# Kernel optimization log

Measured on AMD Instinct MI355X. Metric: run time of the kernel, lower is better.

The kernel has to match this reference:

```python
import jax, jax.numpy as jnp
import numpy as np

N = 20000
E = 320000
D = 512
H = 512


def _gcn_norm(edge_index, num_nodes):
    # PyG GCNConv: add self-loops, then sym-normalize with in-degree of A+I
    src = jnp.concatenate([edge_index[0], jnp.arange(num_nodes)])
    dst = jnp.concatenate([edge_index[1], jnp.arange(num_nodes)])
    deg = jax.ops.segment_sum(jnp.ones_like(dst, dtype=jnp.float32), dst, num_segments=num_nodes)
    dinv = jnp.where(deg > 0, jax.lax.rsqrt(deg), 0.0)
    norm = dinv[src] * dinv[dst]  # [E+N]
    return src, dst, norm


def _gcn_layer(x, src, dst, norm, W, b, num_nodes):
    h = x @ W                          # [N, out]
    msg = h[src] * norm[:, None]       # gather + scale, [E+N, out]
    out = jax.ops.segment_sum(msg, dst, num_segments=num_nodes)  # scatter-add
    return out + b


def setup_inputs() -> dict:
    key = jax.random.key(0)
    ks = jax.random.split(key, 8)
    features = jax.random.normal(ks[0], (N, D), dtype=jnp.float32)
    edge_index = jax.random.randint(ks[1], (2, E), 0, N, dtype=jnp.int64)
    edge_attr = jax.random.normal(ks[2], (E, 1), dtype=jnp.float32)  # unused by GCNConv
    s1 = 1.0 / np.sqrt(D)
    s2 = 1.0 / np.sqrt(H)
    W1 = jax.random.uniform(ks[3], (D, H), dtype=jnp.float32, minval=-s1, maxval=s1)
    b1 = jnp.zeros((H,), dtype=jnp.float32)
    W2 = jax.random.uniform(ks[4], (H, H), dtype=jnp.float32, minval=-s2, maxval=s2)
    b2 = jnp.zeros((H,), dtype=jnp.float32)
    return {"features": features, "edge_index": edge_index, "edge_attr": edge_attr,
            "W1": W1, "b1": b1, "W2": W2, "b2": b2}


def reference(features, edge_index, edge_attr, W1, b1, W2, b2):
    src, dst, norm = _gcn_norm(edge_index, N)
    x = jax.nn.relu(_gcn_layer(features, src, dst, norm, W1, b1, N))
    x = jax.nn.relu(_gcn_layer(x, src, dst, norm, W2, b2, N))
    # global_max_pool over the single graph (batch = all zeros) -> [1, H]
    return jnp.max(x, axis=0, keepdims=True)
```

## Files before the change

### kernel.cpp

```cpp
#include <hip/hip_runtime.h>

#define N_NODES 20000
#define MP      20096
#define N_EDGES 320000
#define DIM     512
#define SCAN_BLOCKS 79
#define FILL_BLOCKS 1250
#define W_BLOCKS    512
#define SORT_BLOCKS 79
#define NBIN 4096
#define MAXP_BLOCKS 256
#define MAXP_ROWS   79

typedef _Float16 half8 __attribute__((ext_vector_type(8)));
typedef float floatx4 __attribute__((ext_vector_type(4)));

#define GLD16(g, l) __builtin_amdgcn_global_load_lds( \
    (const __attribute__((address_space(1))) unsigned int*)(g), \
    (__attribute__((address_space(3))) unsigned int*)(l), 16, 0, 0)

__device__ inline void store8(_Float16* p, const float* v) {
    half8 o;
#pragma unroll
    for (int i = 0; i < 8; ++i) o[i] = (_Float16)v[i];
    *(half8*)p = o;
}
__device__ inline void store8(float* p, const float* v) {
    *(float4*)&p[0] = make_float4(v[0], v[1], v[2], v[3]);
    *(float4*)&p[4] = make_float4(v[4], v[5], v[6], v[7]);
}

__global__ void k_count(const int* __restrict__ dst, int* __restrict__ cnt) {
    int e = blockIdx.x * blockDim.x + threadIdx.x;
    if (e < N_EDGES) atomicAdd(&cnt[dst[e]], 1);
}

__global__ __launch_bounds__(256) void k_scan_a(const int* __restrict__ cnt,
                                                int* __restrict__ bsum) {
    __shared__ int buf[256];
    int gi = blockIdx.x * 256 + threadIdx.x;
    buf[threadIdx.x] = (gi < N_NODES) ? cnt[gi] : 0;
    __syncthreads();
    for (int off = 128; off > 0; off >>= 1) {
        if (threadIdx.x < off) buf[threadIdx.x] += buf[threadIdx.x + off];
        __syncthreads();
    }
    if (threadIdx.x == 0) bsum[blockIdx.x] = buf[0];
}

__global__ __launch_bounds__(128) void k_scan_b(const int* __restrict__ bsum,
                                                int* __restrict__ bbase) {
    __shared__ int buf[128];
    int tid = threadIdx.x;
    int v = (tid < SCAN_BLOCKS) ? bsum[tid] : 0;
    buf[tid] = v;
    __syncthreads();
    for (int off = 1; off < 128; off <<= 1) {
        int t = (tid >= off) ? buf[tid - off] : 0;
        __syncthreads();
        buf[tid] += t;
        __syncthreads();
    }
    if (tid < SCAN_BLOCKS) bbase[tid] = buf[tid] - v;
}

__global__ __launch_bounds__(256) void k_scan_c(const int* __restrict__ cnt,
                                                const int* __restrict__ bbase,
                                                int* __restrict__ offs,
                                                int* __restrict__ cursor,
                                                float* __restrict__ dinv,
                                                int* __restrict__ hist) {
    __shared__ int buf[256];
    __shared__ int lh[NBIN];
    int tid = threadIdx.x;
#pragma unroll
    for (int k = 0; k < NBIN / 256; ++k) lh[tid + k * 256] = 0;
    int gi = blockIdx.x * 256 + tid;
    int v = (gi < N_NODES) ? cnt[gi] : 0;
    buf[tid] = v;
    __syncthreads();
    for (int off = 1; off < 256; off <<= 1) {
        int t = (tid >= off) ? buf[tid - off] : 0;
        __syncthreads();
        buf[tid] += t;
        __syncthreads();
    }
    int base = bbase[blockIdx.x];
    if (gi < N_NODES) {
        int incl = base + buf[tid];
        offs[gi + 1] = incl;
        cursor[gi] = incl - v;
        dinv[gi] = rsqrtf((float)v + 1.0f);
        if (gi == 0) offs[0] = 0;
        int bin = (v > 255 ? 255 : v) * 16 + (gi & 15);
        atomicAdd(&lh[bin], 1);
    } else if (gi < MP) {
        dinv[gi] = 0.f;
    }
    __syncthreads();
#pragma unroll
    for (int k = 0; k < NBIN / 256; ++k) {
        int b2 = tid + k * 256;
        if (lh[b2]) atomicAdd(&hist[b2], lh[b2]);
    }
}

__global__ __launch_bounds__(256) void k_prep(const int* __restrict__ src,
                                              const int* __restrict__ dst,
                                              int* __restrict__ cursor,
                                              int* __restrict__ csr_src,
                                              const float* __restrict__ W1,
                                              const float* __restrict__ W2,
                                              _Float16* __restrict__ Wt1,
                                              _Float16* __restrict__ Wt2,
                                              const int* __restrict__ cnt,
                                              const int* __restrict__ hist,
                                              int* __restrict__ bincur,
                                              int* __restrict__ sorted) {
    int b = blockIdx.x;
    if (b < FILL_BLOCKS) {
        int e = b * 256 + threadIdx.x;
        int d = dst[e];
        int pos = atomicAdd(&cursor[d], 1);
        csr_src[pos] = src[e];
        return;
    }
    if (b < FILL_BLOCKS + W_BLOCKS) {
        int local = b - FILL_BLOCKS;
        int z = local >> 8, t = local & 255;
        const float* W = z ? W2 : W1;
        _Float16* Wt = z ? Wt2 : Wt1;
        __shared__ float tile[32][33];
        int bx = (t & 15) * 32, by = (t >> 4) * 32;
        int x = threadIdx.x & 31, y4 = (threadIdx.x >> 5) * 4;
#pragma unroll
        for (int r = 0; r < 4; ++r)
            tile[y4 + r][x] = W[(size_t)(by + y4 + r) * DIM + bx + x];
        __syncthreads();
#pragma unroll
        for (int r = 0; r < 4; ++r)
            Wt[(size_t)(bx + y4 + r) * DIM + by + x] = (_Float16)tile[x][y4 + r];
        return;
    }
    int sb = b - (FILL_BLOCKS + W_BLOCKS);
    __shared__ int sc[NBIN];
    __shared__ int ps[256];
    int tid = threadIdx.x;
    int tsum = 0;
#pragma unroll
    for (int k = 0; k < NBIN / 256; ++k) {
        int h = hist[tid * (NBIN / 256) + k];
        sc[tid * (NBIN / 256) + k] = tsum;
        tsum += h;
    }
    ps[tid] = tsum;
    __syncthreads();
    for (int off = 1; off < 256; off <<= 1) {
        int t = (tid >= off) ? ps[tid - off] : 0;
        __syncthreads();
        ps[tid] += t;
        __syncthreads();
    }
    int gbase = ps[tid] - tsum;
#pragma unroll
    for (int k = 0; k < NBIN / 256; ++k) sc[tid * (NBIN / 256) + k] += gbase;
    __syncthreads();
    int gi = sb * 256 + tid;
    if (gi < N_NODES) {
        int d = cnt[gi];
        int bin = (d > 255 ? 255 : d) * 16 + (gi & 15);
        int pos = sc[bin] + atomicAdd(&bincur[bin], 1);
        sorted[pos] = gi;
    } else if (gi < MP) {
        sorted[gi] = gi;
    }
}

__global__ __launch_bounds__(256) void k_gemm_f16(const _Float16* __restrict__ A,
                                                  const _Float16* __restrict__ Bt,
                                                  const float* __restrict__ dinv,
                                                  _Float16* __restrict__ G) {
    __shared__ _Float16 As[128 * 32];
    __shared__ _Float16 Bs[128 * 32];

    int t = threadIdx.x;
    int w = t >> 6, lane = t & 63;
    int lm = lane & 15, quad = lane >> 4;
    int m0 = blockIdx.x * 128, n0 = blockIdx.y * 128;
    int wm = (w & 1) * 64, wn = (w >> 1) * 64;

    floatx4 acc[4][4];
#pragma unroll
    for (int i = 0; i < 4; ++i)
#pragma unroll
        for (int j = 0; j < 4; ++j) acc[i][j] = (floatx4){0.f, 0.f, 0.f, 0.f};

    for (int k0 = 0; k0 < DIM; k0 += 32) {
        __syncthreads();
#pragma unroll
        for (int i = 0; i < 2; ++i) {
            int s = i * 256 + t;
            int m = s >> 2, kk = (s & 3) * 8;
            GLD16(A + (size_t)(m0 + m) * DIM + k0 + kk, As + s * 8);
            GLD16(Bt + (size_t)(n0 + m) * DIM + k0 + kk, Bs + s * 8);
        }
        __syncthreads();

        half8 af[4], bf[4];
#pragma unroll
        for (int i = 0; i < 4; ++i)
            af[i] = *(const half8*)&As[(wm + i * 16 + lm) * 32 + quad * 8];
#pragma unroll
        for (int j = 0; j < 4; ++j)
            bf[j] = *(const half8*)&Bs[(wn + j * 16 + lm) * 32 + quad * 8];
#pragma unroll
        for (int i = 0; i < 4; ++i)
#pragma unroll
            for (int j = 0; j < 4; ++j)
                acc[i][j] = __builtin_amdgcn_mfma_f32_16x16x32_f16(af[i], bf[j], acc[i][j], 0, 0, 0);
    }

#pragma unroll
    for (int i = 0; i < 4; ++i)
#pragma unroll
        for (int r = 0; r < 4; ++r) {
            int row = m0 + wm + i * 16 + quad * 4 + r;
            float dd = dinv[row];
#pragma unroll
            for (int j = 0; j < 4; ++j) {
                int col = n0 + wn + j * 16 + lm;
                G[(size_t)row * DIM + col] = (_Float16)(dd * acc[i][j][r]);
            }
        }
}

__global__ __launch_bounds__(256) void k_gemm_f32A(const float* __restrict__ A,
                                                   const _Float16* __restrict__ Bt,
                                                   const float* __restrict__ dinv,
                                                   _Float16* __restrict__ G) {
    __shared__ _Float16 As[128 * 32];
    __shared__ _Float16 Bs[128 * 32];

    int t = threadIdx.x;
    int w = t >> 6, lane = t & 63;
    int lm = lane & 15, quad = lane >> 4;
    int m0 = blockIdx.x * 128, n0 = blockIdx.y * 128;
    int wm = (w & 1) * 64, wn = (w >> 1) * 64;

    floatx4 acc[4][4];
#pragma unroll
    for (int i = 0; i < 4; ++i)
#pragma unroll
        for (int j = 0; j < 4; ++j) acc[i][j] = (floatx4){0.f, 0.f, 0.f, 0.f};

    for (int k0 = 0; k0 < DIM; k0 += 32) {
        __syncthreads();
#pragma unroll
        for (int i = 0; i < 2; ++i) {
            int s = i * 256 + t;
            int m = s >> 2, kk = (s & 3) * 8;
            GLD16(Bt + (size_t)(n0 + m) * DIM + k0 + kk, Bs + s * 8);
        }
#pragma unroll
        for (int i = 0; i < 2; ++i) {
            int s = i * 256 + t;
            int m = s >> 2, kk = (s & 3) * 8;
            int arow = m0 + m;
            half8 h;
            if (arow < N_NODES) {
                float4 a0 = *(const float4*)&A[(size_t)arow * DIM + k0 + kk];
                float4 a1 = *(const float4*)&A[(size_t)arow * DIM + k0 + kk + 4];
                h[0] = (_Float16)a0.x; h[1] = (_Float16)a0.y;
                h[2] = (_Float16)a0.z; h[3] = (_Float16)a0.w;
                h[4] = (_Float16)a1.x; h[5] = (_Float16)a1.y;
                h[6] = (_Float16)a1.z; h[7] = (_Float16)a1.w;
            } else {
#pragma unroll
                for (int q = 0; q < 8; ++q) h[q] = (_Float16)0.f;
            }
            *(half8*)&As[s * 8] = h;
        }
        __syncthreads();

        half8 af[4], bf[4];
#pragma unroll
        for (int i = 0; i < 4; ++i)
            af[i] = *(const half8*)&As[(wm + i * 16 + lm) * 32 + quad * 8];
#pragma unroll
        for (int j = 0; j < 4; ++j)
            bf[j] = *(const half8*)&Bs[(wn + j * 16 + lm) * 32 + quad * 8];
#pragma unroll
        for (int i = 0; i < 4; ++i)
#pragma unroll
            for (int j = 0; j < 4; ++j)
                acc[i][j] = __builtin_amdgcn_mfma_f32_16x16x32_f16(af[i], bf[j], acc[i][j], 0, 0, 0);
    }

#pragma unroll
    for (int i = 0; i < 4; ++i)
#pragma unroll
        for (int r = 0; r < 4; ++r) {
            int row = m0 + wm + i * 16 + quad * 4 + r;
            float dd = dinv[row];
#pragma unroll
            for (int j = 0; j < 4; ++j) {
                int col = n0 + wn + j * 16 + lm;
                G[(size_t)row * DIM + col] = (_Float16)(dd * acc[i][j][r]);
            }
        }
}

template <typename OutT>
__global__ __launch_bounds__(256) void k_agg_t(const _Float16* __restrict__ g,
                                               const float* __restrict__ dinv,
                                               const int* __restrict__ offs,
                                               const int* __restrict__ csr_src,
                                               const int* __restrict__ sorted,
                                               const float* __restrict__ bias,
                                               OutT* __restrict__ out) {
    int chunk = blockIdx.x & 7;
    int grp = blockIdx.x >> 3;
    int w = threadIdx.x >> 6, lane = threadIdx.x & 63;
    int slot = lane >> 3, fg = lane & 7;
    int idx = grp * 32 + w * 8 + slot;
    int node = sorted[idx];
    if ((unsigned)node >= (unsigned)MP) return;
    int fbase = chunk * 64 + fg * 8;
    size_t obase = (size_t)node * DIM + fbase;

    if (node >= N_NODES) {
        float z[8] = {0.f, 0.f, 0.f, 0.f, 0.f, 0.f, 0.f, 0.f};
        store8(&out[obase], z);
        return;
    }

    float acc[8];
    half8 self = *(const half8*)&g[obase];
#pragma unroll
    for (int i = 0; i < 8; ++i) acc[i] = (float)self[i];

    int beg = offs[node], end = offs[node + 1];
    int e = beg;
    for (; e + 8 <= end; e += 8) {
        int s0 = csr_src[e],     s1 = csr_src[e + 1], s2 = csr_src[e + 2], s3 = csr_src[e + 3];
        int s4 = csr_src[e + 4], s5 = csr_src[e + 5], s6 = csr_src[e + 6], s7 = csr_src[e + 7];
        half8 v0 = *(const half8*)&g[(size_t)s0 * DIM + fbase];
        half8 v1 = *(const half8*)&g[(size_t)s1 * DIM + fbase];
        half8 v2 = *(const half8*)&g[(size_t)s2 * DIM + fbase];
        half8 v3 = *(const half8*)&g[(size_t)s3 * DIM + fbase];
        half8 v4 = *(const half8*)&g[(size_t)s4 * DIM + fbase];
        half8 v5 = *(const half8*)&g[(size_t)s5 * DIM + fbase];
        half8 v6 = *(const half8*)&g[(size_t)s6 * DIM + fbase];
        half8 v7 = *(const half8*)&g[(size_t)s7 * DIM + fbase];
#pragma unroll
        for (int i = 0; i < 8; ++i)
            acc[i] += (((float)v0[i] + (float)v1[i]) + ((float)v2[i] + (float)v3[i])) +
                      (((float)v4[i] + (float)v5[i]) + ((float)v6[i] + (float)v7[i]));
    }
    for (; e + 4 <= end; e += 4) {
        int s0 = csr_src[e], s1 = csr_src[e + 1], s2 = csr_src[e + 2], s3 = csr_src[e + 3];
        half8 v0 = *(const half8*)&g[(size_t)s0 * DIM + fbase];
        half8 v1 = *(const half8*)&g[(size_t)s1 * DIM + fbase];
        half8 v2 = *(const half8*)&g[(size_t)s2 * DIM + fbase];
        half8 v3 = *(const half8*)&g[(size_t)s3 * DIM + fbase];
#pragma unroll
        for (int i = 0; i < 8; ++i)
            acc[i] += ((float)v0[i] + (float)v1[i]) + ((float)v2[i] + (float)v3[i]);
    }
    for (; e < end; ++e) {
        int s = csr_src[e];
        half8 v = *(const half8*)&g[(size_t)s * DIM + fbase];
#pragma unroll
        for (int i = 0; i < 8; ++i) acc[i] += (float)v[i];
    }

    float dd = dinv[node];
    float4 b0 = *(const float4*)&bias[fbase];
    float4 b1 = *(const float4*)&bias[fbase + 4];
    float bb[8] = {b0.x, b0.y, b0.z, b0.w, b1.x, b1.y, b1.z, b1.w};
    float o[8];
#pragma unroll
    for (int i = 0; i < 8; ++i) o[i] = fmaxf(fmaf(dd, acc[i], bb[i]), 0.f);
    store8(&out[obase], o);
}

__global__ __launch_bounds__(256) void k_maxpool(const float* __restrict__ x,
                                                 float* __restrict__ out) {
    __shared__ float lmax[4][DIM];
    int stream = threadIdx.x >> 6, lane = threadIdx.x & 63;
    int f0 = lane * 8;
    int r0 = blockIdx.x * MAXP_ROWS;
    int r1 = min(r0 + MAXP_ROWS, N_NODES);

    float m[8];
#pragma unroll
    for (int i = 0; i < 8; ++i) m[i] = 0.f;
    for (int r = r0 + stream; r < r1; r += 4) {
        float4 a = *(const float4*)&x[(size_t)r * DIM + f0];
        float4 b = *(const float4*)&x[(size_t)r * DIM + f0 + 4];
        m[0] = fmaxf(m[0], a.x); m[1] = fmaxf(m[1], a.y);
        m[2] = fmaxf(m[2], a.z); m[3] = fmaxf(m[3], a.w);
        m[4] = fmaxf(m[4], b.x); m[5] = fmaxf(m[5], b.y);
        m[6] = fmaxf(m[6], b.z); m[7] = fmaxf(m[7], b.w);
    }
#pragma unroll
    for (int i = 0; i < 8; ++i) lmax[stream][f0 + i] = m[i];
    __syncthreads();
#pragma unroll
    for (int rep = 0; rep < 2; ++rep) {
        int f = rep * 256 + threadIdx.x;
        float v = fmaxf(fmaxf(lmax[0][f], lmax[1][f]), fmaxf(lmax[2][f], lmax[3][f]));
        atomicMax((int*)&out[f], __float_as_int(v));
    }
}

extern "C" void kernel_launch(void* const* d_in, const int* in_sizes, int n_in,
                              void* d_out, int out_size, void* d_ws, size_t ws_size,
                              hipStream_t stream) {
    const float* features = (const float*)d_in[0];
    const int*   ei       = (const int*)d_in[1];
    const float* W1       = (const float*)d_in[3];
    const float* b1       = (const float*)d_in[4];
    const float* W2       = (const float*)d_in[5];
    const float* b2       = (const float*)d_in[6];
    float* out = (float*)d_out;

    const int* src = ei;
    const int* dst = ei + N_EDGES;

    char* p = (char*)d_ws;
    auto alloc = [&](size_t bytes) { void* r = p; p += (bytes + 255) & ~(size_t)255; return r; };
    int*      cnt    = (int*)alloc(N_NODES * 4);
    int*      hist   = (int*)alloc(NBIN * 4);
    int*      bincur = (int*)alloc(NBIN * 4);
    char*     zeroEnd = p;
    int*      offs   = (int*)alloc((N_NODES + 1) * 4);
    int*      cursor = (int*)alloc(N_NODES * 4);
    float*    dinv   = (float*)alloc(MP * 4);
    int*      csr    = (int*)alloc(N_EDGES * 4);
    int*      bsum   = (int*)alloc(SCAN_BLOCKS * 4);
    int*      bbase  = (int*)alloc(SCAN_BLOCKS * 4);
    int*      sorted = (int*)alloc(MP * 4);
    _Float16* Wt1  = (_Float16*)alloc((size_t)DIM * DIM * 2);
    _Float16* Wt2  = (_Float16*)alloc((size_t)DIM * DIM * 2);
    _Float16* gbuf = (_Float16*)alloc((size_t)MP * DIM * 2);
    _Float16* x1f  = (_Float16*)alloc((size_t)MP * DIM * 2);
    float*    x2f  = (float*)alloc((size_t)MP * DIM * 4);

    hipMemsetAsync(cnt, 0, (size_t)(zeroEnd - (char*)cnt), stream);
    hipMemsetAsync(out, 0, DIM * 4, stream);

    k_count<<<FILL_BLOCKS, 256, 0, stream>>>(dst, cnt);
    k_scan_a<<<SCAN_BLOCKS, 256, 0, stream>>>(cnt, bsum);
    k_scan_b<<<1, 128, 0, stream>>>(bsum, bbase);
    k_scan_c<<<SCAN_BLOCKS, 256, 0, stream>>>(cnt, bbase, offs, cursor, dinv, hist);

    k_prep<<<FILL_BLOCKS + W_BLOCKS + SORT_BLOCKS, 256, 0, stream>>>(
        src, dst, cursor, csr, W1, W2, Wt1, Wt2, cnt, hist, bincur, sorted);

    dim3 ggrd(MP / 128, DIM / 128);

    k_gemm_f32A<<<ggrd, 256, 0, stream>>>(features, Wt1, dinv, gbuf);
    k_agg_t<_Float16><<<8 * (MP / 32), 256, 0, stream>>>(gbuf, dinv, offs, csr, sorted, b1, x1f);

    k_gemm_f16<<<ggrd, 256, 0, stream>>>(x1f, Wt2, dinv, gbuf);
    k_agg_t<float><<<8 * (MP / 32), 256, 0, stream>>>(gbuf, dinv, offs, csr, sorted, b2, x2f);

    k_maxpool<<<MAXP_BLOCKS, 256, 0, stream>>>(x2f, out);
}
```

Before: 271.7 us.

## Fuse second aggregation with global max-pool and prefetch A tiles in GEMM

The second-layer aggregation kernel now reduces its output rows to a per-block column max in shared memory and atomically maxes into the final output. This removes the fp32 x2 buffer write, its read-back, and the separate maxpool launch. Separately, the fp32-input GEMM loads the next K-slice of A into registers during the MFMA loop, so global latency overlaps compute. The prefetch adds register pressure, and the fused kernel adds one atomicMax per column per block.

```diff
diff --git a/kernel.cpp b/kernel.cpp
--- a/kernel.cpp
+++ b/kernel.cpp
@@ -9,8 +9,6 @@
 #define W_BLOCKS    512
 #define SORT_BLOCKS 79
 #define NBIN 4096
-#define MAXP_BLOCKS 256
-#define MAXP_ROWS   79
 
 typedef _Float16 half8 __attribute__((ext_vector_type(8)));
 typedef float floatx4 __attribute__((ext_vector_type(4)));
@@ -18,17 +16,6 @@
 #define GLD16(g, l) __builtin_amdgcn_global_load_lds( \
     (const __attribute__((address_space(1))) unsigned int*)(g), \
     (__attribute__((address_space(3))) unsigned int*)(l), 16, 0, 0)
-
-__device__ inline void store8(_Float16* p, const float* v) {
-    half8 o;
-#pragma unroll
-    for (int i = 0; i < 8; ++i) o[i] = (_Float16)v[i];
-    *(half8*)p = o;
-}
-__device__ inline void store8(float* p, const float* v) {
-    *(float4*)&p[0] = make_float4(v[0], v[1], v[2], v[3]);
-    *(float4*)&p[4] = make_float4(v[4], v[5], v[6], v[7]);
-}
 
 __global__ void k_count(const int* __restrict__ dst, int* __restrict__ cnt) {
     int e = blockIdx.x * blockDim.x + threadIdx.x;
@@ -247,11 +234,24 @@
     int m0 = blockIdx.x * 128, n0 = blockIdx.y * 128;
     int wm = (w & 1) * 64, wn = (w >> 1) * 64;
 
+    int s0 = t, s1 = 256 + t;
+    int am0 = s0 >> 2, ak0 = (s0 & 3) * 8;
+    int am1 = s1 >> 2, ak1 = (s1 & 3) * 8;
+    bool v0 = (m0 + am0) < N_NODES;
+    bool v1 = (m0 + am1) < N_NODES;
+    const float* ap0 = A + (size_t)(m0 + am0) * DIM + ak0;
+    const float* ap1 = A + (size_t)(m0 + am1) * DIM + ak1;
+
     floatx4 acc[4][4];
 #pragma unroll
     for (int i = 0; i < 4; ++i)
 #pragma unroll
         for (int j = 0; j < 4; ++j) acc[i][j] = (floatx4){0.f, 0.f, 0.f, 0.f};
+
+    float4 z4 = make_float4(0.f, 0.f, 0.f, 0.f);
+    float4 p0a = z4, p0b = z4, p1a = z4, p1b = z4;
+    if (v0) { p0a = *(const float4*)(ap0); p0b = *(const float4*)(ap0 + 4); }
+    if (v1) { p1a = *(const float4*)(ap1); p1b = *(const float4*)(ap1 + 4); }
 
     for (int k0 = 0; k0 < DIM; k0 += 32) {
         __syncthreads();
@@ -261,24 +261,18 @@
             int m = s >> 2, kk = (s & 3) * 8;
             GLD16(Bt + (size_t)(n0 + m) * DIM + k0 + kk, Bs + s * 8);
         }
-#pragma unroll
-        for (int i = 0; i < 2; ++i) {
-            int s = i * 256 + t;
-            int m = s >> 2, kk = (s & 3) * 8;
-            int arow = m0 + m;
-            half8 h;
-            if (arow < N_NODES) {
-                float4 a0 = *(const float4*)&A[(size_t)arow * DIM + k0 + kk];
-                float4 a1 = *(const float4*)&A[(size_t)arow * DIM + k0 + kk + 4];
-                h[0] = (_Float16)a0.x; h[1] = (_Float16)a0.y;
-                h[2] = (_Float16)a0.z; h[3] = (_Float16)a0.w;
-                h[4] = (_Float16)a1.x; h[5] = (_Float16)a1.y;
-                h[6] = (_Float16)a1.z; h[7] = (_Float16)a1.w;
-            } else {
-#pragma unroll
-                for (int q = 0; q < 8; ++q) h[q] = (_Float16)0.f;
-            }
-            *(half8*)&As[s * 8] = h;
+        {
+            half8 h0, h1;
+            h0[0] = (_Float16)p0a.x; h0[1] = (_Float16)p0a.y;
+            h0[2] = (_Float16)p0a.z; h0[3] = (_Float16)p0a.w;
+            h0[4] = (_Float16)p0b.x; h0[5] = (_Float16)p0b.y;
+            h0[6] = (_Float16)p0b.z; h0[7] = (_Float16)p0b.w;
+            h1[0] = (_Float16)p1a.x; h1[1] = (_Float16)p1a.y;
+            h1[2] = (_Float16)p1a.z; h1[3] = (_Float16)p1a.w;
+            h1[4] = (_Float16)p1b.x; h1[5] = (_Float16)p1b.y;
+            h1[6] = (_Float16)p1b.z; h1[7] = (_Float16)p1b.w;
+            *(half8*)&As[s0 * 8] = h0;
+            *(half8*)&As[s1 * 8] = h1;
         }
         __syncthreads();
 
@@ -294,6 +288,12 @@
 #pragma unroll
             for (int j = 0; j < 4; ++j)
                 acc[i][j] = __builtin_amdgcn_mfma_f32_16x16x32_f16(af[i], bf[j], acc[i][j], 0, 0, 0);
+
+        int kn = k0 + 32;
+        if (kn < DIM) {
+            if (v0) { p0a = *(const float4*)(ap0 + kn); p0b = *(const float4*)(ap0 + kn + 4); }
+            if (v1) { p1a = *(const float4*)(ap1 + kn); p1b = *(const float4*)(ap1 + kn + 4); }
+        }
     }
 
 #pragma unroll
@@ -310,14 +310,13 @@
         }
 }
 
-template <typename OutT>
-__global__ __launch_bounds__(256) void k_agg_t(const _Float16* __restrict__ g,
-                                               const float* __restrict__ dinv,
-                                               const int* __restrict__ offs,
-                                               const int* __restrict__ csr_src,
-                                               const int* __restrict__ sorted,
-                                               const float* __restrict__ bias,
-                                               OutT* __restrict__ out) {
+__global__ __launch_bounds__(256) void k_agg1(const _Float16* __restrict__ g,
+                                              const float* __restrict__ dinv,
+                                              const int* __restrict__ offs,
+                                              const int* __restrict__ csr_src,
+                                              const int* __restrict__ sorted,
+                                              const float* __restrict__ bias,
+                                              _Float16* __restrict__ out) {
     int chunk = blockIdx.x & 7;
     int grp = blockIdx.x >> 3;
     int w = threadIdx.x >> 6, lane = threadIdx.x & 63;
@@ -329,8 +328,10 @@
     size_t obase = (size_t)node * DIM + fbase;
 
     if (node >= N_NODES) {
-        float z[8] = {0.f, 0.f, 0.f, 0.f, 0.f, 0.f, 0.f, 0.f};
-        store8(&out[obase], z);
+        half8 z;
+#pragma unroll
+        for (int i = 0; i < 8; ++i) z[i] = (_Float16)0.f;
+        *(half8*)&out[obase] = z;
         return;
     }
 
@@ -378,39 +379,95 @@
     float4 b0 = *(const float4*)&bias[fbase];
     float4 b1 = *(const float4*)&bias[fbase + 4];
     float bb[8] = {b0.x, b0.y, b0.z, b0.w, b1.x, b1.y, b1.z, b1.w};
+    half8 o;
+#pragma unroll
+    for (int i = 0; i < 8; ++i) o[i] = (_Float16)fmaxf(fmaf(dd, acc[i], bb[i]), 0.f);
+    *(half8*)&out[obase] = o;
+}
+
+__global__ __launch_bounds__(256) void k_agg_pool(const _Float16* __restrict__ g,
+                                                  const float* __restrict__ dinv,
+                                                  const int* __restrict__ offs,
+                                                  const int* __restrict__ csr_src,
+                                                  const int* __restrict__ sorted,
+                                                  const float* __restrict__ bias,
+                                                  float* __restrict__ out) {
+    __shared__ float lmax[32 * 68];
+    int chunk = blockIdx.x & 7;
+    int grp = blockIdx.x >> 3;
+    int w = threadIdx.x >> 6, lane = threadIdx.x & 63;
+    int slot = lane >> 3, fg = lane & 7;
+    int idx = grp * 32 + w * 8 + slot;
+    int node = sorted[idx];
+    int fbase = chunk * 64 + fg * 8;
+    bool valid = ((unsigned)node < (unsigned)N_NODES);
+
     float o[8];
 #pragma unroll
-    for (int i = 0; i < 8; ++i) o[i] = fmaxf(fmaf(dd, acc[i], bb[i]), 0.f);
-    store8(&out[obase], o);
-}
-
-__global__ __launch_bounds__(256) void k_maxpool(const float* __restrict__ x,
-                                                 float* __restrict__ out) {
-    __shared__ float lmax[4][DIM];
-    int stream = threadIdx.x >> 6, lane = threadIdx.x & 63;
-    int f0 = lane * 8;
-    int r0 = blockIdx.x * MAXP_ROWS;
-    int r1 = min(r0 + MAXP_ROWS, N_NODES);
-
-    float m[8];
-#pragma unroll
-    for (int i = 0; i < 8; ++i) m[i] = 0.f;
-    for (int r = r0 + stream; r < r1; r += 4) {
-        float4 a = *(const float4*)&x[(size_t)r * DIM + f0];
-        float4 b = *(const float4*)&x[(size_t)r * DIM + f0 + 4];
-        m[0] = fmaxf(m[0], a.x); m[1] = fmaxf(m[1], a.y);
-        m[2] = fmaxf(m[2], a.z); m[3] = fmaxf(m[3], a.w);
-        m[4] = fmaxf(m[4], b.x); m[5] = fmaxf(m[5], b.y);
-        m[6] = fmaxf(m[6], b.z); m[7] = fmaxf(m[7], b.w);
-    }
-#pragma unroll
-    for (int i = 0; i < 8; ++i) lmax[stream][f0 + i] = m[i];
-    __syncthreads();
-#pragma unroll
-    for (int rep = 0; rep < 2; ++rep) {
-        int f = rep * 256 + threadIdx.x;
-        float v = fmaxf(fmaxf(lmax[0][f], lmax[1][f]), fmaxf(lmax[2][f], lmax[3][f]));
-        atomicMax((int*)&out[f], __float_as_int(v));
+    for (int i = 0; i < 8; ++i) o[i] = 0.f;
+
+    if (valid) {
+        size_t obase = (size_t)node * DIM + fbase;
+        float acc[8];
+        half8 self = *(const half8*)&g[obase];
+#pragma unroll
+        for (int i = 0; i < 8; ++i) acc[i] = (float)self[i];
+
+        int beg = offs[node], end = offs[node + 1];
+        int e = beg;
+        for (; e + 8 <= end; e += 8) {
+            int s0 = csr_src[e],     s1 = csr_src[e + 1], s2 = csr_src[e + 2], s3 = csr_src[e + 3];
+            int s4 = csr_src[e + 4], s5 = csr_src[e + 5], s6 = csr_src[e + 6], s7 = csr_src[e + 7];
+            half8 v0 = *(const half8*)&g[(size_t)s0 * DIM + fbase];
+            half8 v1 = *(const half8*)&g[(size_t)s1 * DIM + fbase];
+            half8 v2 = *(const half8*)&g[(size_t)s2 * DIM + fbase];
+            half8 v3 = *(const half8*)&g[(size_t)s3 * DIM + fbase];
+            half8 v4 = *(const half8*)&g[(size_t)s4 * DIM + fbase];
+            half8 v5 = *(const half8*)&g[(size_t)s5 * DIM + fbase];
+            half8 v6 = *(const half8*)&g[(size_t)s6 * DIM + fbase];
+            half8 v7 = *(const half8*)&g[(size_t)s7 * DIM + fbase];
+#pragma unroll
+            for (int i = 0; i < 8; ++i)
+                o[i] = (((float)v0[i] + (float)v1[i]) + ((float)v2[i] + (float)v3[i])) +
+                       (((float)v4[i] + (float)v5[i]) + ((float)v6[i] + (float)v7[i]));
+#pragma unroll
+            for (int i = 0; i < 8; ++i) acc[i] += o[i];
+        }
+        for (; e + 4 <= end; e += 4) {
+            int s0 = csr_src[e], s1 = csr_src[e + 1], s2 = csr_src[e + 2], s3 = csr_src[e + 3];
+            half8 v0 = *(const half8*)&g[(size_t)s0 * DIM + fbase];
+            half8 v1 = *(const half8*)&g[(size_t)s1 * DIM + fbase];
+            half8 v2 = *(const half8*)&g[(size_t)s2 * DIM + fbase];
+            half8 v3 = *(const half8*)&g[(size_t)s3 * DIM + fbase];
+#pragma unroll
+            for (int i = 0; i < 8; ++i)
+                acc[i] += ((float)v0[i] + (float)v1[i]) + ((float)v2[i] + (float)v3[i]);
+        }
+        for (; e < end; ++e) {
+            int s = csr_src[e];
+            half8 v = *(const half8*)&g[(size_t)s * DIM + fbase];
+#pragma unroll
+            for (int i = 0; i < 8; ++i) acc[i] += (float)v[i];
+        }
+
+        float dd = dinv[node];
+        float4 b0 = *(const float4*)&bias[fbase];
+        float4 b1 = *(const float4*)&bias[fbase + 4];
+        float bb[8] = {b0.x, b0.y, b0.z, b0.w, b1.x, b1.y, b1.z, b1.w};
+#pragma unroll
+        for (int i = 0; i < 8; ++i) o[i] = fmaxf(fmaf(dd, acc[i], bb[i]), 0.f);
+    }
+
+    int row = w * 8 + slot;
+#pragma unroll
+    for (int i = 0; i < 8; ++i) lmax[row * 68 + fg * 8 + i] = o[i];
+    __syncthreads();
+    if (threadIdx.x < 64) {
+        int c = threadIdx.x;
+        float m = 0.f;
+#pragma unroll
+        for (int r = 0; r < 32; ++r) m = fmaxf(m, lmax[r * 68 + c]);
+        atomicMax((int*)&out[chunk * 64 + c], __float_as_int(m));
     }
 }
 
@@ -445,7 +502,6 @@
     _Float16* Wt2  = (_Float16*)alloc((size_t)DIM * DIM * 2);
     _Float16* gbuf = (_Float16*)alloc((size_t)MP * DIM * 2);
     _Float16* x1f  = (_Float16*)alloc((size_t)MP * DIM * 2);
-    float*    x2f  = (float*)alloc((size_t)MP * DIM * 4);
 
     hipMemsetAsync(cnt, 0, (size_t)(zeroEnd - (char*)cnt), stream);
     hipMemsetAsync(out, 0, DIM * 4, stream);
@@ -461,10 +517,8 @@
     dim3 ggrd(MP / 128, DIM / 128);
 
     k_gemm_f32A<<<ggrd, 256, 0, stream>>>(features, Wt1, dinv, gbuf);
-    k_agg_t<_Float16><<<8 * (MP / 32), 256, 0, stream>>>(gbuf, dinv, offs, csr, sorted, b1, x1f);
+    k_agg1<<<8 * (MP / 32), 256, 0, stream>>>(gbuf, dinv, offs, csr, sorted, b1, x1f);
 
     k_gemm_f16<<<ggrd, 256, 0, stream>>>(x1f, Wt2, dinv, gbuf);
-    k_agg_t<float><<<8 * (MP / 32), 256, 0, stream>>>(gbuf, dinv, offs, csr, sorted, b2, x2f);
-
-    k_maxpool<<<MAXP_BLOCKS, 256, 0, stream>>>(x2f, out);
-}
+    k_agg_pool<<<8 * (MP / 32), 256, 0, stream>>>(gbuf, dinv, offs, csr, sorted, b2, out);
+}
```

New measurement: 250.2 us. -7.9%, faster.
